# Kernel tuning notes

Hardware: AMD Instinct MI355X
Metric: run time of the kernel (lower is better)

Reference implementation:

```python
import jax, jax.numpy as jnp
import numpy as np

VOCAB, EMB, HID, OUT = 100000, 300, 512, 1
B, SEQ = 1, 512


def setup_inputs() -> dict:
    key = jax.random.key(0)
    ks = jax.random.split(key, 8)
    s = 1.0 / np.sqrt(HID)  # torch LSTMCell/Linear init scale
    return {
        "x": jax.random.randint(ks[0], (B, SEQ), 0, VOCAB),
        "h0": jnp.zeros((B, HID), jnp.float32),
        "c0": jnp.zeros((B, HID), jnp.float32),
        "emb_table": jax.random.normal(ks[1], (VOCAB, EMB), jnp.float32) * 0.1,
        "W_ih": jax.random.uniform(ks[2], (4 * HID, EMB), jnp.float32, -s, s),
        "W_hh": jax.random.uniform(ks[3], (4 * HID, HID), jnp.float32, -s, s),
        "b_ih": jax.random.uniform(ks[4], (4 * HID,), jnp.float32, -s, s),
        "b_hh": jax.random.uniform(ks[5], (4 * HID,), jnp.float32, -s, s),
        "fc_w": jax.random.uniform(ks[6], (OUT, HID), jnp.float32, -s, s),
        "fc_b": jax.random.uniform(ks[7], (OUT,), jnp.float32, -s, s),
    }


def reference(x, h0, c0, emb_table, W_ih, W_hh, b_ih, b_hh, fc_w, fc_b):
    embeds = emb_table[x]                      # [B, SEQ, EMB]
    # Faithful to torch: embeds[0][i].view(B, EMB) for i in range(EMB); B == 1.
    steps = embeds[0, :EMB].reshape(EMB, B, EMB)  # [EMB steps, B, EMB]

    def cell(carry, xt):
        h, c = carry
        gates = xt @ W_ih.T + b_ih + h @ W_hh.T + b_hh   # [B, 4*HID]
        i, f, g, o = jnp.split(gates, 4, axis=-1)        # torch gate order i,f,g,o
        i = jax.nn.sigmoid(i)
        f = jax.nn.sigmoid(f)
        g = jnp.tanh(g)
        o = jax.nn.sigmoid(o)
        c = f * c + i * g
        h = o * jnp.tanh(c)
        return (h, c), None

    (h, c), _ = jax.lax.scan(cell, (h0, c0), steps)
    # dropout is identity in eval mode
    out = jax.nn.sigmoid(h @ fc_w.T + fc_b)   # [B, OUT]
    out = out.reshape(B, -1)[:, -1]           # [B]
    return (out, h, c)
```

## Files before the change

### kernel.cpp

```cpp
#include <hip/hip_runtime.h>

#define EMBD 300
#define NSTEP 300
#define HID 512
#define G4 2048
#define TPB 256
#define NWG 32

#define TS2 15
#define NSG 20
#define NRG 8

#define SENTINEL 0xFFC00000u

#define XP_SZ    (NSTEP * G4)
#define HSEQ_OFF XP_SZ

__device__ __forceinline__ float fsig(float x) { return 1.0f / (1.0f + __expf(-x)); }
__device__ __forceinline__ float ftanh(float x) {
    x = fminf(15.0f, fmaxf(-15.0f, x));
    float t = __expf(2.0f * x);
    return (t - 1.0f) / (t + 1.0f);
}

__global__ __launch_bounds__(TPB) void xproj_init_kernel(
    const int* __restrict__ x, const float* __restrict__ h0,
    const float* __restrict__ emb, const float* __restrict__ W_ih,
    const float* __restrict__ b_ih, const float* __restrict__ b_hh,
    float* __restrict__ ws) {
    const int rowg = blockIdx.x;
    const int sg   = blockIdx.y;
    const int tid  = threadIdx.x;
    const int t0   = sg * TS2;
    const int r    = rowg * TPB + tid;

    float* hseq = ws + HSEQ_OFF;

    if (rowg == 0) {
        unsigned* hs = (unsigned*)(hseq + (size_t)(t0 + 1) * HID);
        for (int i = tid; i < TS2 * HID; i += TPB) hs[i] = SENTINEL;
        if (sg == 0) {
            for (int i = tid; i < HID; i += TPB) hseq[i] = h0[i];
        }
    }

    __shared__ float e_lds[TS2][EMBD];
    for (int tt = 0; tt < TS2; ++tt) {
        const float* er = emb + (long long)x[t0 + tt] * EMBD;
        for (int i = tid; i < EMBD; i += TPB) e_lds[tt][i] = er[i];
    }
    __syncthreads();

    float acc[TS2];
    const float bsum = b_ih[r] + b_hh[r];
    #pragma unroll
    for (int tt = 0; tt < TS2; ++tt) acc[tt] = bsum;

    const float* wrow = W_ih + (size_t)r * EMBD;
    for (int e = 0; e < EMBD; e += 4) {
        const float4 w4 = *(const float4*)(wrow + e);
        #pragma unroll
        for (int tt = 0; tt < TS2; ++tt) {
            acc[tt] = fmaf(w4.x, e_lds[tt][e],     acc[tt]);
            acc[tt] = fmaf(w4.y, e_lds[tt][e + 1], acc[tt]);
            acc[tt] = fmaf(w4.z, e_lds[tt][e + 2], acc[tt]);
            acc[tt] = fmaf(w4.w, e_lds[tt][e + 3], acc[tt]);
        }
    }
    #pragma unroll
    for (int tt = 0; tt < TS2; ++tt)
        ws[(size_t)(t0 + tt) * G4 + r] = acc[tt];
}

__global__ __launch_bounds__(TPB, 1) void lstm_scan_kernel(
    const float* __restrict__ c0, const float* __restrict__ W_hh,
    const float* __restrict__ fc_w, const float* __restrict__ fc_b,
    float* __restrict__ ws, float* __restrict__ out) {
    const int tid  = threadIdx.x;
    const int wg   = blockIdx.x;
    const int v    = tid >> 6;
    const int lane = tid & 63;
    const int g    = lane >> 4;
    const int li   = lane & 15;
    const int hidx = wg * 16 + v * 4 + g;

    float* hseq     = ws + HSEQ_OFF;
    const float* xp = ws;

    __shared__ __align__(16) float h_lds[2][576];
    __shared__ float red[256];

    float wreg[4][32];
    #pragma unroll
    for (int gate = 0; gate < 4; ++gate) {
        const float* wr = W_hh + ((size_t)gate * HID + hidx) * HID + li * 32;
        #pragma unroll
        for (int k = 0; k < 32; k += 4) {
            const float4 w4 = *(const float4*)(wr + k);
            wreg[gate][k] = w4.x; wreg[gate][k + 1] = w4.y;
            wreg[gate][k + 2] = w4.z; wreg[gate][k + 3] = w4.w;
        }
    }

    const bool upd = (li == 0);
    float c = upd ? c0[hidx] : 0.0f;

    for (int s = 0; s < NSTEP; ++s) {
        float xi = 0.f, xf = 0.f, xg = 0.f, xo = 0.f;
        if (upd) {
            const float* xpt = xp + (size_t)s * G4 + hidx;
            xi = xpt[0]; xf = xpt[HID]; xg = xpt[2 * HID]; xo = xpt[3 * HID];
        }

        {
            const unsigned long long* slot =
                (const unsigned long long*)(hseq + (size_t)s * HID) + tid;
            unsigned long long hv = __hip_atomic_load(slot, __ATOMIC_RELAXED,
                                                      __HIP_MEMORY_SCOPE_AGENT);
            while ((unsigned)hv == SENTINEL || (unsigned)(hv >> 32) == SENTINEL) {
                __builtin_amdgcn_s_sleep(1);
                hv = __hip_atomic_load(slot, __ATOMIC_RELAXED,
                                       __HIP_MEMORY_SCOPE_AGENT);
            }
            const int i0 = 2 * tid;
            *(float2*)&h_lds[s & 1][i0 + ((i0 >> 5) << 2)] =
                make_float2(__uint_as_float((unsigned)hv),
                            __uint_as_float((unsigned)(hv >> 32)));
        }
        __syncthreads();

        float sums[4];
        const float* hrow = &h_lds[s & 1][li * 36];
        #pragma unroll
        for (int gate = 0; gate < 4; ++gate) {
            float acc = 0.0f;
            #pragma unroll
            for (int k = 0; k < 32; k += 4) {
                const float4 h4 = *(const float4*)(hrow + k);
                acc = fmaf(wreg[gate][k],     h4.x, acc);
                acc = fmaf(wreg[gate][k + 1], h4.y, acc);
                acc = fmaf(wreg[gate][k + 2], h4.z, acc);
                acc = fmaf(wreg[gate][k + 3], h4.w, acc);
            }
            acc += __shfl_xor(acc, 1);
            acc += __shfl_xor(acc, 2);
            acc += __shfl_xor(acc, 4);
            acc += __shfl_xor(acc, 8);
            sums[gate] = acc;
        }

        if (upd) {
            const float iv = fsig(sums[0] + xi);
            const float fv = fsig(sums[1] + xf);
            const float gv = ftanh(sums[2] + xg);
            const float ov = fsig(sums[3] + xo);
            c = fv * c + iv * gv;
            const float h = ov * ftanh(c);
            __hip_atomic_store((unsigned*)(hseq + (size_t)(s + 1) * HID + hidx),
                               __float_as_uint(h),
                               __ATOMIC_RELAXED, __HIP_MEMORY_SCOPE_AGENT);
            if (s == NSTEP - 1) {
                out[1 + hidx] = h;
                out[1 + HID + hidx] = c;
            }
        }
    }

    if (wg == 0) {
        const unsigned long long* slot =
            (const unsigned long long*)(hseq + (size_t)NSTEP * HID) + tid;
        unsigned long long hv = __hip_atomic_load(slot, __ATOMIC_RELAXED,
                                                  __HIP_MEMORY_SCOPE_AGENT);
        while ((unsigned)hv == SENTINEL || (unsigned)(hv >> 32) == SENTINEL) {
            __builtin_amdgcn_s_sleep(1);
            hv = __hip_atomic_load(slot, __ATOMIC_RELAXED,
                                   __HIP_MEMORY_SCOPE_AGENT);
        }
        red[tid] = __uint_as_float((unsigned)hv) * fc_w[2 * tid]
                 + __uint_as_float((unsigned)(hv >> 32)) * fc_w[2 * tid + 1];
        __syncthreads();
        for (int off = 128; off > 0; off >>= 1) {
            if (tid < off) red[tid] += red[tid + off];
            __syncthreads();
        }
        if (tid == 0) out[0] = fsig(red[0] + fc_b[0]);
    }
}

extern "C" void kernel_launch(void* const* d_in, const int* in_sizes, int n_in,
                              void* d_out, int out_size, void* d_ws, size_t ws_size,
                              hipStream_t stream) {
    (void)in_sizes; (void)n_in; (void)out_size; (void)ws_size;
    const int*   x     = (const int*)d_in[0];
    const float* h0    = (const float*)d_in[1];
    const float* c0    = (const float*)d_in[2];
    const float* emb   = (const float*)d_in[3];
    const float* W_ih  = (const float*)d_in[4];
    const float* W_hh  = (const float*)d_in[5];
    const float* b_ih  = (const float*)d_in[6];
    const float* b_hh  = (const float*)d_in[7];
    const float* fc_w  = (const float*)d_in[8];
    const float* fc_b  = (const float*)d_in[9];
    float* out = (float*)d_out;
    float* ws  = (float*)d_ws;

    xproj_init_kernel<<<dim3(NRG, NSG), dim3(TPB), 0, stream>>>(
        x, h0, emb, W_ih, b_ih, b_hh, ws);
    lstm_scan_kernel<<<dim3(NWG), dim3(TPB), 0, stream>>>(
        c0, W_hh, fc_w, fc_b, ws, out);
}
```

Baseline: 719.3 us.

## Replicate scan workgroups with LDS weights and extra publisher wave for h exchange

Launches 256 workgroups instead of 32, with eight redundant copies of each 16-unit slice. Each copy stages its W_hh slice in LDS instead of registers and adds a fifth wave that republishes h with agent-scope stores. Polling now uses sc0 loads via inline asm, with an atomic load every 16th iteration, and barriers become raw s_barrier calls. The redundant writers are meant to spread the cross-workgroup h broadcast and cut polling latency on the serial recurrence, at the cost of much more duplicated compute and global traffic.

```diff
diff --git a/kernel.cpp b/kernel.cpp
--- a/kernel.cpp
+++ b/kernel.cpp
@@ -4,8 +4,10 @@
 #define NSTEP 300
 #define HID 512
 #define G4 2048
-#define TPB 256
-#define NWG 32
+#define TPB1 256
+#define TPB2 320
+#define NCLUST 8
+#define NMEMB 32
 
 #define TS2 15
 #define NSG 20
@@ -23,7 +25,17 @@
     return (t - 1.0f) / (t + 1.0f);
 }
 
-__global__ __launch_bounds__(TPB) void xproj_init_kernel(
+__device__ __forceinline__ unsigned long long load2_sc0(const void* p) {
+    unsigned long long v;
+    asm volatile("global_load_dwordx2 %0, %1, off sc0\n\ts_waitcnt vmcnt(0)"
+                 : "=v"(v) : "v"(p));
+    return v;
+}
+__device__ __forceinline__ void store1_sc0(void* p, unsigned v) {
+    asm volatile("global_store_dword %0, %1, off sc0" :: "v"(p), "v"(v));
+}
+
+__global__ __launch_bounds__(TPB1) void xproj_init_kernel(
     const int* __restrict__ x, const float* __restrict__ h0,
     const float* __restrict__ emb, const float* __restrict__ W_ih,
     const float* __restrict__ b_ih, const float* __restrict__ b_hh,
@@ -32,22 +44,22 @@
     const int sg   = blockIdx.y;
     const int tid  = threadIdx.x;
     const int t0   = sg * TS2;
-    const int r    = rowg * TPB + tid;
+    const int r    = rowg * TPB1 + tid;
 
     float* hseq = ws + HSEQ_OFF;
 
     if (rowg == 0) {
         unsigned* hs = (unsigned*)(hseq + (size_t)(t0 + 1) * HID);
-        for (int i = tid; i < TS2 * HID; i += TPB) hs[i] = SENTINEL;
+        for (int i = tid; i < TS2 * HID; i += TPB1) hs[i] = SENTINEL;
         if (sg == 0) {
-            for (int i = tid; i < HID; i += TPB) hseq[i] = h0[i];
+            for (int i = tid; i < HID; i += TPB1) hseq[i] = h0[i];
         }
     }
 
     __shared__ float e_lds[TS2][EMBD];
     for (int tt = 0; tt < TS2; ++tt) {
         const float* er = emb + (long long)x[t0 + tt] * EMBD;
-        for (int i = tid; i < EMBD; i += TPB) e_lds[tt][i] = er[i];
+        for (int i = tid; i < EMBD; i += TPB1) e_lds[tt][i] = er[i];
     }
     __syncthreads();
 
@@ -72,112 +84,144 @@
         ws[(size_t)(t0 + tt) * G4 + r] = acc[tt];
 }
 
-__global__ __launch_bounds__(TPB, 1) void lstm_scan_kernel(
+__global__ __launch_bounds__(TPB2, 1) void lstm_scan_kernel(
     const float* __restrict__ c0, const float* __restrict__ W_hh,
     const float* __restrict__ fc_w, const float* __restrict__ fc_b,
     float* __restrict__ ws, float* __restrict__ out) {
     const int tid  = threadIdx.x;
-    const int wg   = blockIdx.x;
+    const int wgid = blockIdx.x;
+    const int m    = wgid >> 3;
     const int v    = tid >> 6;
     const int lane = tid & 63;
     const int g    = lane >> 4;
     const int li   = lane & 15;
-    const int hidx = wg * 16 + v * 4 + g;
+    const int hidx4 = v * 4 + g;
+    const int hidx  = m * 16 + hidx4;
 
     float* hseq     = ws + HSEQ_OFF;
     const float* xp = ws;
 
+    __shared__ __align__(16) float wlds[16 * 4 * 8 * 16 * 4];
     __shared__ __align__(16) float h_lds[2][576];
+    __shared__ float hpub[16];
     __shared__ float red[256];
 
-    float wreg[4][32];
-    #pragma unroll
-    for (int gate = 0; gate < 4; ++gate) {
-        const float* wr = W_hh + ((size_t)gate * HID + hidx) * HID + li * 32;
-        #pragma unroll
-        for (int k = 0; k < 32; k += 4) {
-            const float4 w4 = *(const float4*)(wr + k);
-            wreg[gate][k] = w4.x; wreg[gate][k + 1] = w4.y;
-            wreg[gate][k + 2] = w4.z; wreg[gate][k + 3] = w4.w;
-        }
-    }
-
-    const bool upd = (li == 0);
-    float c = upd ? c0[hidx] : 0.0f;
-
-    for (int s = 0; s < NSTEP; ++s) {
-        float xi = 0.f, xf = 0.f, xg = 0.f, xo = 0.f;
-        if (upd) {
-            const float* xpt = xp + (size_t)s * G4 + hidx;
-            xi = xpt[0]; xf = xpt[HID]; xg = xpt[2 * HID]; xo = xpt[3 * HID];
-        }
-
-        {
-            const unsigned long long* slot =
-                (const unsigned long long*)(hseq + (size_t)s * HID) + tid;
-            unsigned long long hv = __hip_atomic_load(slot, __ATOMIC_RELAXED,
-                                                      __HIP_MEMORY_SCOPE_AGENT);
-            while ((unsigned)hv == SENTINEL || (unsigned)(hv >> 32) == SENTINEL) {
-                __builtin_amdgcn_s_sleep(1);
-                hv = __hip_atomic_load(slot, __ATOMIC_RELAXED,
-                                       __HIP_MEMORY_SCOPE_AGENT);
-            }
-            const int i0 = 2 * tid;
-            *(float2*)&h_lds[s & 1][i0 + ((i0 >> 5) << 2)] =
-                make_float2(__uint_as_float((unsigned)hv),
-                            __uint_as_float((unsigned)(hv >> 32)));
-        }
-        __syncthreads();
-
-        float sums[4];
-        const float* hrow = &h_lds[s & 1][li * 36];
+    if (v < 4) {
         #pragma unroll
         for (int gate = 0; gate < 4; ++gate) {
-            float acc = 0.0f;
+            const float* wr = W_hh + ((size_t)gate * HID + hidx) * HID + li * 32;
             #pragma unroll
-            for (int k = 0; k < 32; k += 4) {
-                const float4 h4 = *(const float4*)(hrow + k);
-                acc = fmaf(wreg[gate][k],     h4.x, acc);
-                acc = fmaf(wreg[gate][k + 1], h4.y, acc);
-                acc = fmaf(wreg[gate][k + 2], h4.z, acc);
-                acc = fmaf(wreg[gate][k + 3], h4.w, acc);
-            }
-            acc += __shfl_xor(acc, 1);
-            acc += __shfl_xor(acc, 2);
-            acc += __shfl_xor(acc, 4);
-            acc += __shfl_xor(acc, 8);
-            sums[gate] = acc;
-        }
-
-        if (upd) {
-            const float iv = fsig(sums[0] + xi);
-            const float fv = fsig(sums[1] + xf);
-            const float gv = ftanh(sums[2] + xg);
-            const float ov = fsig(sums[3] + xo);
-            c = fv * c + iv * gv;
-            const float h = ov * ftanh(c);
-            __hip_atomic_store((unsigned*)(hseq + (size_t)(s + 1) * HID + hidx),
-                               __float_as_uint(h),
-                               __ATOMIC_RELAXED, __HIP_MEMORY_SCOPE_AGENT);
-            if (s == NSTEP - 1) {
-                out[1 + hidx] = h;
-                out[1 + HID + hidx] = c;
-            }
-        }
-    }
-
-    if (wg == 0) {
-        const unsigned long long* slot =
-            (const unsigned long long*)(hseq + (size_t)NSTEP * HID) + tid;
-        unsigned long long hv = __hip_atomic_load(slot, __ATOMIC_RELAXED,
-                                                  __HIP_MEMORY_SCOPE_AGENT);
-        while ((unsigned)hv == SENTINEL || (unsigned)(hv >> 32) == SENTINEL) {
-            __builtin_amdgcn_s_sleep(1);
-            hv = __hip_atomic_load(slot, __ATOMIC_RELAXED,
-                                   __HIP_MEMORY_SCOPE_AGENT);
-        }
-        red[tid] = __uint_as_float((unsigned)hv) * fc_w[2 * tid]
-                 + __uint_as_float((unsigned)(hv >> 32)) * fc_w[2 * tid + 1];
+            for (int k4 = 0; k4 < 8; ++k4) {
+                *(float4*)&wlds[((((hidx4 * 4) + gate) * 8 + k4) * 16 + li) * 4] =
+                    *(const float4*)(wr + k4 * 4);
+            }
+        }
+    }
+    __syncthreads();
+
+    const bool upd = (v < 4) && (li == 0);
+    float c = upd ? c0[hidx] : 0.0f;
+
+    for (int s = 0; s < NSTEP; ++s) {
+        if (v < 4) {
+            float xi = 0.f, xf = 0.f, xg = 0.f, xo = 0.f;
+            if (upd) {
+                const float* xpt = xp + (size_t)s * G4 + hidx;
+                xi = xpt[0]; xf = xpt[HID]; xg = xpt[2 * HID]; xo = xpt[3 * HID];
+            }
+
+            {
+                const unsigned long long* slot =
+                    (const unsigned long long*)(hseq + (size_t)s * HID) + tid;
+                unsigned long long hv = load2_sc0(slot);
+                int k = 0;
+                while ((unsigned)hv == SENTINEL || (unsigned)(hv >> 32) == SENTINEL) {
+                    if ((++k & 15) == 0)
+                        hv = __hip_atomic_load(slot, __ATOMIC_RELAXED,
+                                               __HIP_MEMORY_SCOPE_AGENT);
+                    else
+                        hv = load2_sc0(slot);
+                }
+                const int i0 = 2 * tid;
+                *(float2*)&h_lds[s & 1][i0 + ((i0 >> 5) << 2)] =
+                    make_float2(__uint_as_float((unsigned)hv),
+                                __uint_as_float((unsigned)(hv >> 32)));
+            }
+            asm volatile("s_waitcnt lgkmcnt(0)");
+            __builtin_amdgcn_s_barrier();
+
+            float4 hreg[8];
+            const float* hrow = &h_lds[s & 1][li * 36];
+            #pragma unroll
+            for (int k4 = 0; k4 < 8; ++k4) hreg[k4] = *(const float4*)(hrow + k4 * 4);
+
+            float a0 = 0.f, a1 = 0.f, a2 = 0.f, a3 = 0.f;
+            #pragma unroll
+            for (int k4 = 0; k4 < 8; ++k4) {
+                const float4 h4 = hreg[k4];
+                const float4 w0 = *(const float4*)&wlds[(((hidx4 * 4 + 0) * 8 + k4) * 16 + li) * 4];
+                const float4 w1 = *(const float4*)&wlds[(((hidx4 * 4 + 1) * 8 + k4) * 16 + li) * 4];
+                const float4 w2 = *(const float4*)&wlds[(((hidx4 * 4 + 2) * 8 + k4) * 16 + li) * 4];
+                const float4 w3 = *(const float4*)&wlds[(((hidx4 * 4 + 3) * 8 + k4) * 16 + li) * 4];
+                a0 = fmaf(w0.x, h4.x, a0); a0 = fmaf(w0.y, h4.y, a0);
+                a0 = fmaf(w0.z, h4.z, a0); a0 = fmaf(w0.w, h4.w, a0);
+                a1 = fmaf(w1.x, h4.x, a1); a1 = fmaf(w1.y, h4.y, a1);
+                a1 = fmaf(w1.z, h4.z, a1); a1 = fmaf(w1.w, h4.w, a1);
+                a2 = fmaf(w2.x, h4.x, a2); a2 = fmaf(w2.y, h4.y, a2);
+                a2 = fmaf(w2.z, h4.z, a2); a2 = fmaf(w2.w, h4.w, a2);
+                a3 = fmaf(w3.x, h4.x, a3); a3 = fmaf(w3.y, h4.y, a3);
+                a3 = fmaf(w3.z, h4.z, a3); a3 = fmaf(w3.w, h4.w, a3);
+            }
+            #define RED16(A) A += __shfl_xor(A, 1); A += __shfl_xor(A, 2); \
+                             A += __shfl_xor(A, 4); A += __shfl_xor(A, 8);
+            RED16(a0) RED16(a1) RED16(a2) RED16(a3)
+            #undef RED16
+
+            if (upd) {
+                const float iv = fsig(a0 + xi);
+                const float fv = fsig(a1 + xf);
+                const float gv = ftanh(a2 + xg);
+                const float ov = fsig(a3 + xo);
+                c = fv * c + iv * gv;
+                const float h = ov * ftanh(c);
+                store1_sc0((unsigned*)(hseq + (size_t)(s + 1) * HID + hidx),
+                           __float_as_uint(h));
+                hpub[hidx4] = h;
+                if (s == NSTEP - 1) {
+                    out[1 + hidx] = h;
+                    out[1 + HID + hidx] = c;
+                }
+            }
+            asm volatile("s_waitcnt lgkmcnt(0)");
+            __builtin_amdgcn_s_barrier();
+        } else {
+            __builtin_amdgcn_s_barrier();
+            __builtin_amdgcn_s_barrier();
+            if (lane < 16) {
+                const float h = hpub[lane];
+                __hip_atomic_store((unsigned*)(hseq + (size_t)(s + 1) * HID + m * 16 + lane),
+                                   __float_as_uint(h),
+                                   __ATOMIC_RELAXED, __HIP_MEMORY_SCOPE_AGENT);
+            }
+        }
+    }
+
+    if (m == 0) {
+        if (tid < 256) {
+            const unsigned long long* slot =
+                (const unsigned long long*)(hseq + (size_t)NSTEP * HID) + tid;
+            unsigned long long hv = load2_sc0(slot);
+            int k = 0;
+            while ((unsigned)hv == SENTINEL || (unsigned)(hv >> 32) == SENTINEL) {
+                if ((++k & 15) == 0)
+                    hv = __hip_atomic_load(slot, __ATOMIC_RELAXED,
+                                           __HIP_MEMORY_SCOPE_AGENT);
+                else
+                    hv = load2_sc0(slot);
+            }
+            red[tid] = __uint_as_float((unsigned)hv) * fc_w[2 * tid]
+                     + __uint_as_float((unsigned)(hv >> 32)) * fc_w[2 * tid + 1];
+        }
         __syncthreads();
         for (int off = 128; off > 0; off >>= 1) {
             if (tid < off) red[tid] += red[tid + off];
@@ -204,8 +248,8 @@
     float* out = (float*)d_out;
     float* ws  = (float*)d_ws;
 
-    xproj_init_kernel<<<dim3(NRG, NSG), dim3(TPB), 0, stream>>>(
+    xproj_init_kernel<<<dim3(NRG, NSG), dim3(TPB1), 0, stream>>>(
         x, h0, emb, W_ih, b_ih, b_hh, ws);
-    lstm_scan_kernel<<<dim3(NWG), dim3(TPB), 0, stream>>>(
+    lstm_scan_kernel<<<dim3(NCLUST * NMEMB), dim3(TPB2), 0, stream>>>(
         c0, W_hh, fc_w, fc_b, ws, out);
 }
```

After: 1.078 ms. 1.5x slower.
